# Kernel tuning notes

Hardware: AMD Instinct MI355X
Metric: run time of the kernel (lower is better)

Reference implementation:

```python
import jax, jax.numpy as jnp
import numpy as np

D_MODEL = 1024
N_SH = 16            # sub-heads per branch
N_BR = 4             # branches
H_TOT = N_BR * N_SH  # 64 total heads
DH = D_MODEL // N_SH # 64 head dim
BRANCH_CONFIGS = [(16, 0), (128, 16), (128, 0), (512, 144)]


def rms_norm(x):
    eps = jnp.finfo(x.dtype).eps
    return x * jax.lax.rsqrt(jnp.mean(x * x, axis=-1, keepdims=True) + eps)


def rope(x):
    # x: [B, H, T, Dh]; non-standard RoPE: even/odd split, halves concatenated
    T, Dh = x.shape[2], x.shape[3]
    inv_freq = 1.0 / (10000.0 ** (jnp.arange(0, Dh, 2, dtype=jnp.float32) / Dh))
    freqs = jnp.arange(T, dtype=jnp.float32)[:, None] * inv_freq[None, :]  # [T, Dh/2]
    cos = jnp.cos(freqs)[None, None]
    sin = jnp.sin(freqs)[None, None]
    x1 = x[..., 0::2]
    x2 = x[..., 1::2]
    return jnp.concatenate([-x2 * sin + x1 * cos, x1 * sin + x2 * cos], axis=-1)


def setup_inputs() -> dict:
    key = jax.random.key(0)
    ks = jax.random.split(key, 12)
    B, T, C = 2, 1024, D_MODEL
    s = 0.02
    return {
        "X": jax.random.normal(ks[0], (B, T, C), jnp.float32),
        "WQ": jax.random.normal(ks[1], (C, H_TOT * DH), jnp.float32) * s,
        "bQ": jax.random.normal(ks[2], (H_TOT * DH,), jnp.float32) * s,
        "WK": jax.random.normal(ks[3], (C, C), jnp.float32) * s,
        "bK": jax.random.normal(ks[4], (C,), jnp.float32) * s,
        "WV": jax.random.normal(ks[5], (C, H_TOT * DH), jnp.float32) * s,
        "bV": jax.random.normal(ks[6], (H_TOT * DH,), jnp.float32) * s,
        "WO": jax.random.normal(ks[7], (C, C), jnp.float32) * s,
        "bO": jax.random.normal(ks[8], (C,), jnp.float32) * s,
        "sink_scalars": jax.random.normal(ks[9], (H_TOT,), jnp.float32) * s,
        "v_nulls": jax.random.normal(ks[10], (H_TOT, DH), jnp.float32) * s,
    }


def reference(X, WQ, bQ, WK, bK, WV, bV, WO, bO, sink_scalars, v_nulls):
    B, T, C = X.shape
    # projections -> [B, H, T, Dh]
    q = (X @ WQ + bQ).reshape(B, T, H_TOT, DH).transpose(0, 2, 1, 3)
    q = rope(rms_norm(q))
    v = (X @ WV + bV).reshape(B, T, H_TOT, DH).transpose(0, 2, 1, 3)
    k = rope((X @ WK + bK).reshape(B, T, N_SH, DH).transpose(0, 2, 1, 3))
    k = jnp.tile(k, (1, N_BR, 1, 1))  # [B, H_TOT, T, Dh]

    # KMax scores with key self-norm denominator
    scores = jnp.einsum('bhqd,bhkd->bhqk', q, k)
    denom = jnp.sqrt(jnp.sum(k * k, axis=-1))[:, :, None, :]  # [B,H,1,T]
    w = scores / denom

    # banded masks per branch; note: off-band logits become 0 (NOT -inf) -> exp(0)=1 in softmax
    idx = jnp.arange(T)
    dist = idx[:, None] - idx[None, :]  # query - key
    bmasks = jnp.stack([((dist >= g) & (dist < h)).astype(w.dtype)
                        for (h, g) in BRANCH_CONFIGS], axis=0)  # [N_BR,T,T]
    full_mask = jnp.repeat(bmasks, N_SH, axis=0)[None]  # [1,H_TOT,T,T] (band subset of tril)
    w = w * full_mask

    # learnable tanh sink logit per head, concatenated as extra column
    sinks = jnp.broadcast_to(jnp.tanh(sink_scalars).reshape(1, H_TOT, 1, 1), (B, H_TOT, T, 1))
    probs = jax.nn.softmax(jnp.concatenate([w, sinks], axis=-1), axis=-1)

    out = jnp.einsum('bhqk,bhkd->bhqd', probs[..., :T], v)
    out = out + probs[..., T:] * v_nulls.reshape(1, H_TOT, 1, DH)

    # [B,H_TOT,T,Dh] -> [B,N_BR,T,C]
    ctx = out.reshape(B, N_BR, N_SH, T, DH).transpose(0, 1, 3, 2, 4).reshape(B, N_BR, T, C)
    y = ctx @ WO + bO
    return y.mean(axis=1)
```

## Files before the change

### kernel.cpp

```cpp
#include <hip/hip_runtime.h>
#include <hip/hip_bf16.h>
#include <math.h>

#define T_SEQ 1024
#define LOG2_10000 13.287712379549449f

typedef unsigned short u16;
typedef unsigned int u32;
typedef __attribute__((ext_vector_type(8))) short bf16x8;
typedef __attribute__((ext_vector_type(4))) float f32x4;

__device__ __forceinline__ void gload16(const u16* g, const u16* s) {
  __builtin_amdgcn_global_load_lds(
      (const __attribute__((address_space(1))) void*)g,
      (__attribute__((address_space(3))) void*)s, 16, 0, 0);
}

__device__ __forceinline__ u16 f2bf(float x) {
  __hip_bfloat16 h = __float2bfloat16(x);
  return *reinterpret_cast<u16*>(&h);
}
__device__ __forceinline__ float bf2f(u16 x) {
  __hip_bfloat16 h = *reinterpret_cast<__hip_bfloat16*>(&x);
  return __bfloat162float(h);
}

__device__ __forceinline__ void transpose_step(
    const float* __restrict__ W, u16* __restrict__ Wt, int N, int nbx,
    int local, int t, float (*tile)[33]) {
  int bx = local % nbx, by = local / nbx;
  int n0 = bx * 32, k0 = by * 32;
  int r = t >> 3, c4 = (t & 7) * 4;
  float4 v = *reinterpret_cast<const float4*>(&W[(size_t)(k0 + r) * N + n0 + c4]);
  tile[r][c4 + 0] = v.x;
  tile[r][c4 + 1] = v.y;
  tile[r][c4 + 2] = v.z;
  tile[r][c4 + 3] = v.w;
  __syncthreads();
  u16 o[4];
#pragma unroll
  for (int i = 0; i < 4; ++i) o[i] = f2bf(tile[c4 + i][r]);
  *reinterpret_cast<uint2*>(&Wt[(size_t)(n0 + r) * 1024 + k0 + c4]) =
      *reinterpret_cast<const uint2*>(o);
}

__global__ __launch_bounds__(256) void prep_kernel(
    const float* __restrict__ X, const float* __restrict__ WQ,
    const float* __restrict__ WK, const float* __restrict__ WV,
    const float* __restrict__ WO, const float* __restrict__ bQ,
    const float* __restrict__ bV, const float* __restrict__ bK,
    u16* __restrict__ Xb, u16* __restrict__ WQVKt, u16* __restrict__ WOt,
    float* __restrict__ bQVK, float* __restrict__ ctab, float* __restrict__ stab)
{
  __shared__ float tile[32][33];
  const int blk = blockIdx.x, t = threadIdx.x;
  if (blk < 128) {
    int id = blk * 256 + t;
    int tt = id >> 5, p = id & 31;
    float invf = exp2f(-LOG2_10000 * (float)(2 * p) * (1.0f / 64.0f));
    float ang = (float)tt * invf;
    float sn, cs;
    sincosf(ang, &sn, &cs);
    ctab[id] = cs;
    stab[id] = sn;
  } else if (blk < 1152) {
    int i = (blk - 128) * 256 + t;
    float4 a = reinterpret_cast<const float4*>(X)[2 * i];
    float4 b = reinterpret_cast<const float4*>(X)[2 * i + 1];
    u16 o[8] = {f2bf(a.x), f2bf(a.y), f2bf(a.z), f2bf(a.w),
                f2bf(b.x), f2bf(b.y), f2bf(b.z), f2bf(b.w)};
    reinterpret_cast<uint4*>(Xb)[i] = *reinterpret_cast<const uint4*>(o);
  } else if (blk < 5248) {
    transpose_step(WQ, WQVKt, 4096, 128, blk - 1152, t, tile);
  } else if (blk < 9344) {
    transpose_step(WV, WQVKt + (size_t)4096 * 1024, 4096, 128, blk - 5248, t, tile);
  } else if (blk < 10368) {
    transpose_step(WK, WQVKt + (size_t)8192 * 1024, 1024, 32, blk - 9344, t, tile);
  } else if (blk < 11392) {
    transpose_step(WO, WOt, 1024, 32, blk - 10368, t, tile);
  } else {
    int id = (blk - 11392) * 256 + t;
    if (id < 9216)
      bQVK[id] = (id < 4096) ? bQ[id] : (id < 8192) ? bV[id - 4096] : bK[id - 8192];
  }
}

__global__ __launch_bounds__(512, 4) void gemm_qv_kernel(
    const u16* __restrict__ Ab, const u16* __restrict__ Bt,
    const float* __restrict__ bias, u16* __restrict__ Cqv)
{
  __shared__ __align__(16) u16 sA[3][256 * 32];
  __shared__ __align__(16) u16 sB[3][128 * 32];

  const int tid = threadIdx.x;
  const int lane = tid & 63;
  const int w = tid >> 6;
  const int wm = w >> 2, wn = w & 3;
  const int l15 = lane & 15, l4 = lane >> 4;

  const int orig = blockIdx.x;
  const int xcd = orig & 7, j = orig >> 3;
  const int bx = xcd * 8 + (j & 7);
  const int by = j >> 3;
  const int m0 = by * 256, n0 = bx * 128;

  const int rA0 = tid >> 2, cA = tid & 3;
  const int scA = cA ^ ((rA0 >> 1) & 3);
  const int rB0 = tid >> 2;
  const int scB = cA ^ ((rB0 >> 1) & 3);
  const u16* aA0 = Ab + (size_t)(m0 + rA0) * 1024 + 8 * scA;
  const u16* aA1 = Ab + (size_t)(m0 + rA0 + 128) * 1024 + 8 * scA;
  const u16* aB0 = Bt + (size_t)(n0 + rB0) * 1024 + 8 * scB;

  const int cp = l4 ^ ((l15 >> 1) & 3);

  f32x4 acc[8][2];
#pragma unroll
  for (int i = 0; i < 8; ++i)
#pragma unroll
    for (int jn = 0; jn < 2; ++jn) acc[i][jn] = (f32x4){0.f, 0.f, 0.f, 0.f};

#define STAGE(t)                                                               \
  {                                                                            \
    const int sl = (t) % 3;                                                    \
    const int ko = (t) * 32;                                                   \
    gload16(aA0 + ko, &sA[sl][tid * 8]);                                       \
    gload16(aA1 + ko, &sA[sl][4096 + tid * 8]);                                \
    gload16(aB0 + ko, &sB[sl][tid * 8]);                                       \
  }

  STAGE(0);
#pragma unroll 1
  for (int t = 0; t < 32; ++t) {
    if (t + 1 < 32) {
      STAGE(t + 1);
      asm volatile("s_waitcnt vmcnt(3)" ::: "memory");
    } else {
      asm volatile("s_waitcnt vmcnt(0)" ::: "memory");
    }
    __builtin_amdgcn_sched_barrier(0);
    __builtin_amdgcn_s_barrier();
    __builtin_amdgcn_sched_barrier(0);

    const u16* tA = sA[t % 3];
    const u16* tB = sB[t % 3];

    bf16x8 bf[2];
#pragma unroll
    for (int n = 0; n < 2; ++n) {
      int row = wn * 32 + n * 16 + l15;
      bf[n] = *reinterpret_cast<const bf16x8*>(&tB[row * 32 + cp * 8]);
    }
    bf16x8 af[8];
#pragma unroll
    for (int m = 0; m < 8; ++m) {
      int row = wm * 128 + m * 16 + l15;
      af[m] = *reinterpret_cast<const bf16x8*>(&tA[row * 32 + cp * 8]);
    }
    __builtin_amdgcn_s_setprio(1);
#pragma unroll
    for (int m = 0; m < 8; ++m)
#pragma unroll
      for (int n = 0; n < 2; ++n)
        acc[m][n] = __builtin_amdgcn_mfma_f32_16x16x32_bf16(
            af[m], bf[n], acc[m][n], 0, 0, 0);
    __builtin_amdgcn_s_setprio(0);
  }
#undef STAGE

#pragma unroll
  for (int n = 0; n < 2; ++n) {
    int col = n0 + wn * 32 + n * 16 + l15;
    float bv = bias[col];
#pragma unroll
    for (int mf = 0; mf < 8; ++mf) {
#pragma unroll
      for (int r = 0; r < 4; ++r) {
        int row = m0 + wm * 128 + mf * 16 + l4 * 4 + r;
        Cqv[(size_t)row * 8192 + col] = f2bf(acc[mf][n][r] + bv);
      }
    }
  }
}

template <bool BF16OUT>
__global__ __launch_bounds__(256) void gemm64_kernel(
    const u16* __restrict__ Ab, const u16* __restrict__ Bt,
    const float* __restrict__ bias, void* __restrict__ Cv,
    int M, int N, int K)
{
  __shared__ __align__(16) u16 sA[2][64 * 64];
  __shared__ __align__(16) u16 sB[2][64 * 64];
  const int tid = threadIdx.x;
  const int lane = tid & 63;
  const int wv = tid >> 6;
  const int wm = wv >> 1, wn = wv & 1;
  const int l15 = lane & 15, l4 = lane >> 4;
  const int m0 = blockIdx.y * 64, n0 = blockIdx.x * 64;

  f32x4 acc[2][2];
#pragma unroll
  for (int i = 0; i < 2; ++i)
#pragma unroll
    for (int j = 0; j < 2; ++j) acc[i][j] = (f32x4){0.f, 0.f, 0.f, 0.f};

  const int r0s = tid >> 3,         c0s = tid & 7;
  const int r1s = (256 + tid) >> 3, c1s = (256 + tid) & 7;
  const int sc0 = c0s ^ (r0s & 7);
  const int sc1 = c1s ^ (r1s & 7);
  const u16* aA0 = Ab + (size_t)(m0 + r0s) * K + 8 * sc0;
  const u16* aA1 = Ab + (size_t)(m0 + r1s) * K + 8 * sc1;
  const u16* aB0 = Bt + (size_t)(n0 + r0s) * K + 8 * sc0;
  const u16* aB1 = Bt + (size_t)(n0 + r1s) * K + 8 * sc1;

  gload16(aA0, &sA[0][tid * 8]);
  gload16(aA1, &sA[0][2048 + tid * 8]);
  gload16(aB0, &sB[0][tid * 8]);
  gload16(aB1, &sB[0][2048 + tid * 8]);

  const int niter = K >> 6;
#pragma unroll 1
  for (int it = 0; it < niter; ++it) {
    const int buf = it & 1;
    __builtin_amdgcn_s_barrier();
    if (it + 1 < niter) {
      const int ko = (it + 1) * 64;
      gload16(aA0 + ko, &sA[buf ^ 1][tid * 8]);
      gload16(aA1 + ko, &sA[buf ^ 1][2048 + tid * 8]);
      gload16(aB0 + ko, &sB[buf ^ 1][tid * 8]);
      gload16(aB1 + ko, &sB[buf ^ 1][2048 + tid * 8]);
      asm volatile("s_waitcnt vmcnt(4)" ::: "memory");
    } else {
      asm volatile("s_waitcnt vmcnt(0)" ::: "memory");
    }
    __builtin_amdgcn_sched_barrier(0);
    bf16x8 af[2][2], bfv[2][2];
#pragma unroll
    for (int kk = 0; kk < 2; ++kk) {
#pragma unroll
      for (int mi = 0; mi < 2; ++mi) {
        int row = wm * 32 + mi * 16 + l15;
        int cs = (kk * 4 + l4) ^ (row & 7);
        af[mi][kk] = *reinterpret_cast<const bf16x8*>(&sA[buf][row * 64 + cs * 8]);
      }
#pragma unroll
      for (int ni = 0; ni < 2; ++ni) {
        int row = wn * 32 + ni * 16 + l15;
        int cs = (kk * 4 + l4) ^ (row & 7);
        bfv[ni][kk] = *reinterpret_cast<const bf16x8*>(&sB[buf][row * 64 + cs * 8]);
      }
    }
#pragma unroll
    for (int kk = 0; kk < 2; ++kk)
#pragma unroll
      for (int mi = 0; mi < 2; ++mi)
#pragma unroll
        for (int ni = 0; ni < 2; ++ni)
          acc[mi][ni] = __builtin_amdgcn_mfma_f32_16x16x32_bf16(
              af[mi][kk], bfv[ni][kk], acc[mi][ni], 0, 0, 0);
  }

#pragma unroll
  for (int mi = 0; mi < 2; ++mi)
#pragma unroll
    for (int ni = 0; ni < 2; ++ni) {
      int col = n0 + wn * 32 + ni * 16 + l15;
      float bv = bias[col];
#pragma unroll
      for (int r = 0; r < 4; ++r) {
        int row = m0 + wm * 32 + mi * 16 + l4 * 4 + r;
        float val = acc[mi][ni][r] + bv;
        size_t idx = (size_t)row * N + col;
        if (BF16OUT) ((u16*)Cv)[idx] = f2bf(val);
        else ((float*)Cv)[idx] = val;
      }
    }
}

__global__ __launch_bounds__(256) void qkvt_kernel(
    u16* __restrict__ QVbf, u16* __restrict__ Kbf,
    const float* __restrict__ ctab, const float* __restrict__ stab,
    float* __restrict__ part)
{
  const int blk = blockIdx.x;
  if (blk < 20480) {
    const int rid  = blk * 8 + (threadIdx.x >> 5);
    const int lane = threadIdx.x & 63;
    const int p    = lane & 31;
    const int gb   = lane & 32;

    u16* row;
    int t;
    const bool isQ = rid < 131072;
    if (isQ) {
      int h = rid & 63, bt = rid >> 6;
      t = bt & 1023;
      row = QVbf + (size_t)bt * 8192 + h * 64;
    } else {
      int r2 = rid - 131072;
      int hsL = r2 & 15, bt = r2 >> 4;
      t = bt & 1023;
      row = Kbf + (size_t)bt * 1024 + hsL * 64;
    }

    u32 v = reinterpret_cast<const u32*>(row)[p];
    float x1 = bf2f((u16)v), x2 = bf2f((u16)(v >> 16));
    float cs = ctab[t * 32 + p], sn = stab[t * 32 + p];

    float o_lo, o_hi;
    if (isQ) {
      float ss = x1 * x1 + x2 * x2;
      ss += __shfl_xor(ss, 1, 64);
      ss += __shfl_xor(ss, 2, 64);
      ss += __shfl_xor(ss, 4, 64);
      ss += __shfl_xor(ss, 8, 64);
      ss += __shfl_xor(ss, 16, 64);
      float rs = rsqrtf(ss * (1.0f / 64.0f) + 1.1920929e-7f);
      float xn1 = x1 * rs, xn2 = x2 * rs;
      o_lo = xn1 * cs - xn2 * sn;
      o_hi = xn1 * sn + xn2 * cs;
    } else {
      float xr1 = x1 * cs - x2 * sn;
      float xr2 = x1 * sn + x2 * cs;
      float ss = xr1 * xr1 + xr2 * xr2;
      ss += __shfl_xor(ss, 1, 64);
      ss += __shfl_xor(ss, 2, 64);
      ss += __shfl_xor(ss, 4, 64);
      ss += __shfl_xor(ss, 8, 64);
      ss += __shfl_xor(ss, 16, 64);
      float rs = rsqrtf(ss);
      o_lo = xr1 * rs;
      o_hi = xr2 * rs;
    }

    int m = (2 * p) & 31;
    float slo0 = __shfl(o_lo, gb + m, 64);
    float slo1 = __shfl(o_lo, gb + m + 1, 64);
    float shi0 = __shfl(o_hi, gb + m, 64);
    float shi1 = __shfl(o_hi, gb + m + 1, 64);
    float e0 = (p < 16) ? slo0 : shi0;
    float e1 = (p < 16) ? slo1 : shi1;
    reinterpret_cast<u32*>(row)[p] = (u32)f2bf(e0) | ((u32)f2bf(e1) << 16);
  } else {
    int vb = blk - 20480;
    int b = vb >> 6, ch = vb & 63;
    const u16* base = QVbf + (size_t)(b * 1024 + ch * 16) * 8192 + 4096;
#pragma unroll
    for (int g = 0; g < 2; ++g) {
      int c0 = (threadIdx.x + g * 256) * 8;
      float s[8] = {0.f, 0.f, 0.f, 0.f, 0.f, 0.f, 0.f, 0.f};
#pragma unroll 4
      for (int r = 0; r < 16; ++r) {
        bf16x8 v = *reinterpret_cast<const bf16x8*>(&base[(size_t)r * 8192 + c0]);
#pragma unroll
        for (int e = 0; e < 8; ++e) s[e] += bf2f((u16)v[e]);
      }
      float* dst = &part[(size_t)vb * 4096 + c0];
#pragma unroll
      for (int e = 0; e < 8; ++e) dst[e] = s[e];
    }
  }
}

__global__ __launch_bounds__(256) void vsum_reduce_kernel(
    const float* __restrict__ part, float* __restrict__ Vsum) {
  int id = blockIdx.x * 256 + threadIdx.x;
  int b = id >> 12, n = id & 4095;
  float s = 0.f;
#pragma unroll 8
  for (int ch = 0; ch < 64; ++ch) s += part[(size_t)(b * 64 + ch) * 4096 + n];
  Vsum[id] = s;
}

__global__ __launch_bounds__(256) void attn_mfma_kernel(
    const u16* __restrict__ Qv, const u16* __restrict__ Kb,
    const float* __restrict__ Vsum, const float* __restrict__ sink,
    const float* __restrict__ vnull, u16* __restrict__ mctxb)
{
  __shared__ __align__(16) u16 sQ[64 * 64];
  __shared__ __align__(16) u16 sK[2][64 * 64];
  __shared__ __align__(16) u16 sVt[2][64 * 64];
  __shared__ __align__(16) u16 sP[64 * 64];

  int blk = blockIdx.x;
  blk = (blk & 7) * 64 + (blk >> 3);
  const int qt  = blk & 15;
  const int hs  = (blk >> 4) & 15;
  const int b   = blk >> 8;
  const int qt0 = qt * 64;

  const int tid  = threadIdx.x;
  const int lane = tid & 63;
  const int wv   = tid >> 6;
  const int l15  = lane & 15;
  const int l4   = lane >> 4;
  const int qr0  = tid >> 3, qi0 = tid & 7;
  const int qr1  = qr0 + 32;
  const int vjp  = tid & 31, vdg = tid >> 5;
  const int qrow = wv * 16 + l15;

  constexpr int HCFG[4] = {16, 128, 128, 512};
  constexpr int GCFG[4] = {0, 16, 0, 144};

  f32x4 macc[4];
#pragma unroll
  for (int i = 0; i < 4; ++i) macc[i] = (f32x4){0.f, 0.f, 0.f, 0.f};

#pragma unroll 1
  for (int br = 0; br < 4; ++br) {
    const int h = br * 16 + hs;
    const int hmax = HCFG[br], g = GCFG[br];
    int klo = qt0 - (hmax - 1); if (klo < 0) klo = 0;
    int khi = qt0 + 63 - g;     if (khi > 1023) khi = 1023;
    const int nc = (khi >= klo) ? ((khi - klo) / 64 + 1) : 0;

    gload16(Qv + (size_t)(b * 1024 + qt0 + qr0) * 8192 + h * 64 + 8 * (qi0 ^ (qr0 & 7)),
            sQ + (size_t)wv * 512);
    gload16(Qv + (size_t)(b * 1024 + qt0 + qr1) * 8192 + h * 64 + 8 * (qi0 ^ (qr1 & 7)),
            sQ + 2048 + (size_t)wv * 512);
    bf16x8 va, vb;
    if (nc > 0) {
      int ja0 = klo + qr0; if (ja0 > 1023) ja0 = 1023;
      int ja1 = klo + qr1; if (ja1 > 1023) ja1 = 1023;
      gload16(Kb + (size_t)(b * 1024 + ja0) * 1024 + hs * 64 + 8 * (qi0 ^ (qr0 & 7)),
              sK[0] + (size_t)wv * 512);
      gload16(Kb + (size_t)(b * 1024 + ja1) * 1024 + hs * 64 + 8 * (qi0 ^ (qr1 & 7)),
              sK[0] + 2048 + (size_t)wv * 512);
      int jva = klo + 2 * vjp, jvb = jva + 1;
      if (jva > 1023) jva = 1023;
      if (jvb > 1023) jvb = 1023;
      va = *reinterpret_cast<const bf16x8*>(
          &Qv[(size_t)(b * 1024 + jva) * 8192 + 4096 + h * 64 + vdg * 8]);
      vb = *reinterpret_cast<const bf16x8*>(
          &Qv[(size_t)(b * 1024 + jvb) * 8192 + 4096 + h * 64 + vdg * 8]);
    }
    asm volatile("s_waitcnt vmcnt(0)" ::: "memory");
    __builtin_amdgcn_sched_barrier(0);
    if (nc > 0) {
#pragma unroll
      for (int e = 0; e < 8; ++e) {
        int d = vdg * 8 + e;
        u32 pack = (u32)(u16)va[e] | ((u32)(u16)vb[e] << 16);
        *reinterpret_cast<u32*>(
            (char*)sVt[0] + d * 128 + ((4 * vjp) ^ ((d & 7) << 4))) = pack;
      }
    }
    asm volatile("s_waitcnt lgkmcnt(0)" ::: "memory");
    __builtin_amdgcn_sched_barrier(0);
    __builtin_amdgcn_s_barrier();

    bf16x8 afQ[2];
#pragma unroll
    for (int kh = 0; kh < 2; ++kh) {
      int cs = (4 * kh + l4) ^ (l15 & 7);
      afQ[kh] = *reinterpret_cast<const bf16x8*>(&sQ[qrow * 64 + cs * 8]);
    }

    f32x4 outv[4];
#pragma unroll
    for (int i = 0; i < 4; ++i) outv[i] = (f32x4){0.f, 0.f, 0.f, 0.f};
    float zacc[4] = {0.f, 0.f, 0.f, 0.f};

    int buf = 0;
#pragma unroll 1
    for (int c = 0; c < nc; ++c) {
      const int j0 = klo + c * 64;
      const bool nxt = (c + 1 < nc);
      if (nxt) {
        int j0n = j0 + 64;
        int ja0 = j0n + qr0; if (ja0 > 1023) ja0 = 1023;
        int ja1 = j0n + qr1; if (ja1 > 1023) ja1 = 1023;
        gload16(Kb + (size_t)(b * 1024 + ja0) * 1024 + hs * 64 + 8 * (qi0 ^ (qr0 & 7)),
                sK[buf ^ 1] + (size_t)wv * 512);
        gload16(Kb + (size_t)(b * 1024 + ja1) * 1024 + hs * 64 + 8 * (qi0 ^ (qr1 & 7)),
                sK[buf ^ 1] + 2048 + (size_t)wv * 512);
        int jva = j0n + 2 * vjp, jvb = jva + 1;
        if (jva > 1023) jva = 1023;
        if (jvb > 1023) jvb = 1023;
        va = *reinterpret_cast<const bf16x8*>(
            &Qv[(size_t)(b * 1024 + jva) * 8192 + 4096 + h * 64 + vdg * 8]);
        vb = *reinterpret_cast<const bf16x8*>(
            &Qv[(size_t)(b * 1024 + jvb) * 8192 + 4096 + h * 64 + vdg * 8]);
      }
      f32x4 sfr[4];
      __builtin_amdgcn_s_setprio(1);
#pragma unroll
      for (int jt = 0; jt < 4; ++jt) {
        int krow = jt * 16 + l15;
        f32x4 acc = (f32x4){0.f, 0.f, 0.f, 0.f};
#pragma unroll
        for (int kh = 0; kh < 2; ++kh) {
          int cs = (4 * kh + l4) ^ (l15 & 7);
          bf16x8 bk = *reinterpret_cast<const bf16x8*>(&sK[buf][krow * 64 + cs * 8]);
          acc = __builtin_amdgcn_mfma_f32_16x16x32_bf16(afQ[kh], bk, acc, 0, 0, 0);
        }
        sfr[jt] = acc;
      }
      __builtin_amdgcn_s_setprio(0);
#pragma unroll
      for (int jt = 0; jt < 4; ++jt) {
        int jloc = jt * 16 + l15;
        int jabs = j0 + jloc;
#pragma unroll
        for (int r = 0; r < 4; ++r) {
          int q_r = wv * 16 + l4 * 4 + r;
          int dist = (qt0 + q_r) - jabs;
          bool inband = (dist >= g) & (dist < hmax) & (jabs < 1024);
          float pv = inband ? (__expf(sfr[jt][r]) - 1.0f) : 0.0f;
          zacc[r] += pv;
          *reinterpret_cast<u16*>(
              (char*)sP + q_r * 128 + ((2 * jloc) ^ ((q_r & 7) << 4))) = f2bf(pv);
        }
      }
      asm volatile("s_waitcnt lgkmcnt(0)" ::: "memory");
      __builtin_amdgcn_sched_barrier(0);
      bf16x8 afP[2];
#pragma unroll
      for (int kh = 0; kh < 2; ++kh) {
        int cs = (4 * kh + l4) ^ (l15 & 7);
        afP[kh] = *reinterpret_cast<const bf16x8*>(&sP[qrow * 64 + cs * 8]);
      }
      __builtin_amdgcn_s_setprio(1);
#pragma unroll
      for (int dt = 0; dt < 4; ++dt) {
        int drow = dt * 16 + l15;
#pragma unroll
        for (int kh = 0; kh < 2; ++kh) {
          int cs = (4 * kh + l4) ^ (l15 & 7);
          bf16x8 bv = *reinterpret_cast<const bf16x8*>(&sVt[buf][drow * 64 + cs * 8]);
          outv[dt] = __builtin_amdgcn_mfma_f32_16x16x32_bf16(afP[kh], bv, outv[dt], 0, 0, 0);
        }
      }
      __builtin_amdgcn_s_setprio(0);
      if (nxt) {
#pragma unroll
        for (int e = 0; e < 8; ++e) {
          int d = vdg * 8 + e;
          u32 pack = (u32)(u16)va[e] | ((u32)(u16)vb[e] << 16);
          *reinterpret_cast<u32*>(
              (char*)sVt[buf ^ 1] + d * 128 + ((4 * vjp) ^ ((d & 7) << 4))) = pack;
        }
      }
      asm volatile("s_waitcnt vmcnt(0) lgkmcnt(0)" ::: "memory");
      __builtin_amdgcn_sched_barrier(0);
      __builtin_amdgcn_s_barrier();
      buf ^= 1;
    }

#pragma unroll
    for (int r = 0; r < 4; ++r) {
      zacc[r] += __shfl_xor(zacc[r], 1, 64);
      zacc[r] += __shfl_xor(zacc[r], 2, 64);
      zacc[r] += __shfl_xor(zacc[r], 4, 64);
      zacc[r] += __shfl_xor(zacc[r], 8, 64);
    }
    float es = __expf(tanhf(sink[h]));
#pragma unroll
    for (int dt = 0; dt < 4; ++dt) {
      int d = dt * 16 + l15;
      float vs = Vsum[(size_t)b * 4096 + h * 64 + d];
      float vn = vnull[h * 64 + d];
#pragma unroll
      for (int r = 0; r < 4; ++r) {
        float invZ = 1.0f / (1024.0f + zacc[r] + es);
        macc[dt][r] += (outv[dt][r] + vs + es * vn) * invZ;
      }
    }
  }

#pragma unroll
  for (int dt = 0; dt < 4; ++dt) {
#pragma unroll
    for (int r = 0; r < 4; ++r) {
      int q_r = wv * 16 + l4 * 4 + r;
      mctxb[(size_t)(b * 1024 + qt0 + q_r) * 1024 + hs * 64 + dt * 16 + l15] =
          f2bf(0.25f * macc[dt][r]);
    }
  }
}

extern "C" void kernel_launch(void* const* d_in, const int* in_sizes, int n_in,
                              void* d_out, int out_size, void* d_ws, size_t ws_size,
                              hipStream_t stream) {
  (void)in_sizes; (void)n_in; (void)out_size; (void)ws_size;
  const float* X    = (const float*)d_in[0];
  const float* WQ   = (const float*)d_in[1];
  const float* bQ   = (const float*)d_in[2];
  const float* WK   = (const float*)d_in[3];
  const float* bK   = (const float*)d_in[4];
  const float* WV   = (const float*)d_in[5];
  const float* bV   = (const float*)d_in[6];
  const float* WO   = (const float*)d_in[7];
  const float* bO   = (const float*)d_in[8];
  const float* sink = (const float*)d_in[9];
  const float* vnul = (const float*)d_in[10];
  float* Y = (float*)d_out;

  char* p = (char*)d_ws;
  u16*   Xb    = (u16*)p;   p += (size_t)2048 * 1024 * 2;
  u16*   WQVKt = (u16*)p;   p += (size_t)9216 * 1024 * 2;
  u16*   WOt   = (u16*)p;   p += (size_t)1024 * 1024 * 2;
  u16*   QVbf  = (u16*)p;   p += (size_t)2048 * 8192 * 2;
  u16*   Kbf   = (u16*)p;   p += (size_t)2048 * 1024 * 2;
  u16*   mctxb = (u16*)p;   p += (size_t)2048 * 1024 * 2;
  float* Vsum  = (float*)p; p += (size_t)2 * 4096 * 4;
  float* vpart = (float*)p; p += (size_t)128 * 4096 * 4;
  float* bQVK  = (float*)p; p += (size_t)9216 * 4;
  float* ctab  = (float*)p; p += (size_t)32768 * 4;
  float* stab  = (float*)p; p += (size_t)32768 * 4;

  dim3 blk(256);
  prep_kernel<<<11428, blk, 0, stream>>>(X, WQ, WK, WV, WO, bQ, bV, bK,
                                         Xb, WQVKt, WOt, bQVK, ctab, stab);

  gemm_qv_kernel<<<512, dim3(512), 0, stream>>>(Xb, WQVKt, bQVK, QVbf);
  gemm64_kernel<true><<<dim3(16, 32), blk, 0, stream>>>(
      Xb, WQVKt + (size_t)8192 * 1024, bQVK + 8192, Kbf, 2048, 1024, 1024);

  qkvt_kernel<<<20608, blk, 0, stream>>>(QVbf, Kbf, ctab, stab, vpart);
  vsum_reduce_kernel<<<32, blk, 0, stream>>>(vpart, Vsum);

  attn_mfma_kernel<<<512, blk, 0, stream>>>(QVbf, Kbf, Vsum, sink, vnul, mctxb);

  gemm64_kernel<false><<<dim3(16, 32), blk, 0, stream>>>(mctxb, WOt, bO, Y, 2048, 1024, 1024);
}
```

Measured before the change: 132.2 us.

## Split attention across branches into separate blocks with a merge kernel

The attention kernel now launches one block per (batch, head-slot, query tile, branch) instead of looping over all four branches inside a block. That gives four times as many blocks and better load balance across CUs, since branch 3 has far more key chunks than the others. Each block writes its per-branch bf16 partial to a new workspace buffer, and a separate merge kernel sums the four partials into the context. The cost is an extra launch, extra global memory traffic, and one more bf16 rounding step before the sum.

```diff
diff --git a/kernel.cpp b/kernel.cpp
--- a/kernel.cpp
+++ b/kernel.cpp
@@ -375,7 +375,7 @@
 __global__ __launch_bounds__(256) void attn_mfma_kernel(
     const u16* __restrict__ Qv, const u16* __restrict__ Kb,
     const float* __restrict__ Vsum, const float* __restrict__ sink,
-    const float* __restrict__ vnull, u16* __restrict__ mctxb)
+    const float* __restrict__ vnull, u16* __restrict__ mpart)
 {
   __shared__ __align__(16) u16 sQ[64 * 64];
   __shared__ __align__(16) u16 sK[2][64 * 64];
@@ -383,10 +383,11 @@
   __shared__ __align__(16) u16 sP[64 * 64];
 
   int blk = blockIdx.x;
-  blk = (blk & 7) * 64 + (blk >> 3);
-  const int qt  = blk & 15;
-  const int hs  = (blk >> 4) & 15;
-  const int b   = blk >> 8;
+  blk = (blk & 7) * 256 + (blk >> 3);
+  const int br  = blk & 3;
+  const int qt  = (blk >> 2) & 15;
+  const int hs  = (blk >> 6) & 15;
+  const int b   = blk >> 10;
   const int qt0 = qt * 64;
 
   const int tid  = threadIdx.x;
@@ -402,31 +403,73 @@
   constexpr int HCFG[4] = {16, 128, 128, 512};
   constexpr int GCFG[4] = {0, 16, 0, 144};
 
-  f32x4 macc[4];
-#pragma unroll
-  for (int i = 0; i < 4; ++i) macc[i] = (f32x4){0.f, 0.f, 0.f, 0.f};
-
+  const int h = br * 16 + hs;
+  const int hmax = HCFG[br], g = GCFG[br];
+  int klo = qt0 - (hmax - 1); if (klo < 0) klo = 0;
+  int khi = qt0 + 63 - g;     if (khi > 1023) khi = 1023;
+  const int nc = (khi >= klo) ? ((khi - klo) / 64 + 1) : 0;
+
+  gload16(Qv + (size_t)(b * 1024 + qt0 + qr0) * 8192 + h * 64 + 8 * (qi0 ^ (qr0 & 7)),
+          sQ + (size_t)wv * 512);
+  gload16(Qv + (size_t)(b * 1024 + qt0 + qr1) * 8192 + h * 64 + 8 * (qi0 ^ (qr1 & 7)),
+          sQ + 2048 + (size_t)wv * 512);
+  bf16x8 va, vb;
+  if (nc > 0) {
+    int ja0 = klo + qr0; if (ja0 > 1023) ja0 = 1023;
+    int ja1 = klo + qr1; if (ja1 > 1023) ja1 = 1023;
+    gload16(Kb + (size_t)(b * 1024 + ja0) * 1024 + hs * 64 + 8 * (qi0 ^ (qr0 & 7)),
+            sK[0] + (size_t)wv * 512);
+    gload16(Kb + (size_t)(b * 1024 + ja1) * 1024 + hs * 64 + 8 * (qi0 ^ (qr1 & 7)),
+            sK[0] + 2048 + (size_t)wv * 512);
+    int jva = klo + 2 * vjp, jvb = jva + 1;
+    if (jva > 1023) jva = 1023;
+    if (jvb > 1023) jvb = 1023;
+    va = *reinterpret_cast<const bf16x8*>(
+        &Qv[(size_t)(b * 1024 + jva) * 8192 + 4096 + h * 64 + vdg * 8]);
+    vb = *reinterpret_cast<const bf16x8*>(
+        &Qv[(size_t)(b * 1024 + jvb) * 8192 + 4096 + h * 64 + vdg * 8]);
+  }
+  asm volatile("s_waitcnt vmcnt(0)" ::: "memory");
+  __builtin_amdgcn_sched_barrier(0);
+  if (nc > 0) {
+#pragma unroll
+    for (int e = 0; e < 8; ++e) {
+      int d = vdg * 8 + e;
+      u32 pack = (u32)(u16)va[e] | ((u32)(u16)vb[e] << 16);
+      *reinterpret_cast<u32*>(
+          (char*)sVt[0] + d * 128 + ((4 * vjp) ^ ((d & 7) << 4))) = pack;
+    }
+  }
+  asm volatile("s_waitcnt lgkmcnt(0)" ::: "memory");
+  __builtin_amdgcn_sched_barrier(0);
+  __builtin_amdgcn_s_barrier();
+
+  bf16x8 afQ[2];
+#pragma unroll
+  for (int kh = 0; kh < 2; ++kh) {
+    int cs = (4 * kh + l4) ^ (l15 & 7);
+    afQ[kh] = *reinterpret_cast<const bf16x8*>(&sQ[qrow * 64 + cs * 8]);
+  }
+
+  f32x4 outv[4];
+#pragma unroll
+  for (int i = 0; i < 4; ++i) outv[i] = (f32x4){0.f, 0.f, 0.f, 0.f};
+  float zacc[4] = {0.f, 0.f, 0.f, 0.f};
+
+  int buf = 0;
 #pragma unroll 1
-  for (int br = 0; br < 4; ++br) {
-    const int h = br * 16 + hs;
-    const int hmax = HCFG[br], g = GCFG[br];
-    int klo = qt0 - (hmax - 1); if (klo < 0) klo = 0;
-    int khi = qt0 + 63 - g;     if (khi > 1023) khi = 1023;
-    const int nc = (khi >= klo) ? ((khi - klo) / 64 + 1) : 0;
-
-    gload16(Qv + (size_t)(b * 1024 + qt0 + qr0) * 8192 + h * 64 + 8 * (qi0 ^ (qr0 & 7)),
-            sQ + (size_t)wv * 512);
-    gload16(Qv + (size_t)(b * 1024 + qt0 + qr1) * 8192 + h * 64 + 8 * (qi0 ^ (qr1 & 7)),
-            sQ + 2048 + (size_t)wv * 512);
-    bf16x8 va, vb;
-    if (nc > 0) {
-      int ja0 = klo + qr0; if (ja0 > 1023) ja0 = 1023;
-      int ja1 = klo + qr1; if (ja1 > 1023) ja1 = 1023;
+  for (int c = 0; c < nc; ++c) {
+    const int j0 = klo + c * 64;
+    const bool nxt = (c + 1 < nc);
+    if (nxt) {
+      int j0n = j0 + 64;
+      int ja0 = j0n + qr0; if (ja0 > 1023) ja0 = 1023;
+      int ja1 = j0n + qr1; if (ja1 > 1023) ja1 = 1023;
       gload16(Kb + (size_t)(b * 1024 + ja0) * 1024 + hs * 64 + 8 * (qi0 ^ (qr0 & 7)),
-              sK[0] + (size_t)wv * 512);
+              sK[buf ^ 1] + (size_t)wv * 512);
       gload16(Kb + (size_t)(b * 1024 + ja1) * 1024 + hs * 64 + 8 * (qi0 ^ (qr1 & 7)),
-              sK[0] + 2048 + (size_t)wv * 512);
-      int jva = klo + 2 * vjp, jvb = jva + 1;
+              sK[buf ^ 1] + 2048 + (size_t)wv * 512);
+      int jva = j0n + 2 * vjp, jvb = jva + 1;
       if (jva > 1023) jva = 1023;
       if (jvb > 1023) jvb = 1023;
       va = *reinterpret_cast<const bf16x8*>(
@@ -434,149 +477,112 @@
       vb = *reinterpret_cast<const bf16x8*>(
           &Qv[(size_t)(b * 1024 + jvb) * 8192 + 4096 + h * 64 + vdg * 8]);
     }
-    asm volatile("s_waitcnt vmcnt(0)" ::: "memory");
+    f32x4 sfr[4];
+    __builtin_amdgcn_s_setprio(1);
+#pragma unroll
+    for (int jt = 0; jt < 4; ++jt) {
+      int krow = jt * 16 + l15;
+      f32x4 acc = (f32x4){0.f, 0.f, 0.f, 0.f};
+#pragma unroll
+      for (int kh = 0; kh < 2; ++kh) {
+        int cs = (4 * kh + l4) ^ (l15 & 7);
+        bf16x8 bk = *reinterpret_cast<const bf16x8*>(&sK[buf][krow * 64 + cs * 8]);
+        acc = __builtin_amdgcn_mfma_f32_16x16x32_bf16(afQ[kh], bk, acc, 0, 0, 0);
+      }
+      sfr[jt] = acc;
+    }
+    __builtin_amdgcn_s_setprio(0);
+#pragma unroll
+    for (int jt = 0; jt < 4; ++jt) {
+      int jloc = jt * 16 + l15;
+      int jabs = j0 + jloc;
+#pragma unroll
+      for (int r = 0; r < 4; ++r) {
+        int q_r = wv * 16 + l4 * 4 + r;
+        int dist = (qt0 + q_r) - jabs;
+        bool inband = (dist >= g) & (dist < hmax) & (jabs < 1024);
+        float pv = inband ? (__expf(sfr[jt][r]) - 1.0f) : 0.0f;
+        zacc[r] += pv;
+        *reinterpret_cast<u16*>(
+            (char*)sP + q_r * 128 + ((2 * jloc) ^ ((q_r & 7) << 4))) = f2bf(pv);
+      }
+    }
+    asm volatile("s_waitcnt lgkmcnt(0)" ::: "memory");
     __builtin_amdgcn_sched_barrier(0);
-    if (nc > 0) {
+    bf16x8 afP[2];
+#pragma unroll
+    for (int kh = 0; kh < 2; ++kh) {
+      int cs = (4 * kh + l4) ^ (l15 & 7);
+      afP[kh] = *reinterpret_cast<const bf16x8*>(&sP[qrow * 64 + cs * 8]);
+    }
+    __builtin_amdgcn_s_setprio(1);
+#pragma unroll
+    for (int dt = 0; dt < 4; ++dt) {
+      int drow = dt * 16 + l15;
+#pragma unroll
+      for (int kh = 0; kh < 2; ++kh) {
+        int cs = (4 * kh + l4) ^ (l15 & 7);
+        bf16x8 bv = *reinterpret_cast<const bf16x8*>(&sVt[buf][drow * 64 + cs * 8]);
+        outv[dt] = __builtin_amdgcn_mfma_f32_16x16x32_bf16(afP[kh], bv, outv[dt], 0, 0, 0);
+      }
+    }
+    __builtin_amdgcn_s_setprio(0);
+    if (nxt) {
 #pragma unroll
       for (int e = 0; e < 8; ++e) {
         int d = vdg * 8 + e;
         u32 pack = (u32)(u16)va[e] | ((u32)(u16)vb[e] << 16);
         *reinterpret_cast<u32*>(
-            (char*)sVt[0] + d * 128 + ((4 * vjp) ^ ((d & 7) << 4))) = pack;
-      }
-    }
-    asm volatile("s_waitcnt lgkmcnt(0)" ::: "memory");
+            (char*)sVt[buf ^ 1] + d * 128 + ((4 * vjp) ^ ((d & 7) << 4))) = pack;
+      }
+    }
+    asm volatile("s_waitcnt vmcnt(0) lgkmcnt(0)" ::: "memory");
     __builtin_amdgcn_sched_barrier(0);
     __builtin_amdgcn_s_barrier();
-
-    bf16x8 afQ[2];
-#pragma unroll
-    for (int kh = 0; kh < 2; ++kh) {
-      int cs = (4 * kh + l4) ^ (l15 & 7);
-      afQ[kh] = *reinterpret_cast<const bf16x8*>(&sQ[qrow * 64 + cs * 8]);
-    }
-
-    f32x4 outv[4];
-#pragma unroll
-    for (int i = 0; i < 4; ++i) outv[i] = (f32x4){0.f, 0.f, 0.f, 0.f};
-    float zacc[4] = {0.f, 0.f, 0.f, 0.f};
-
-    int buf = 0;
-#pragma unroll 1
-    for (int c = 0; c < nc; ++c) {
-      const int j0 = klo + c * 64;
-      const bool nxt = (c + 1 < nc);
-      if (nxt) {
-        int j0n = j0 + 64;
-        int ja0 = j0n + qr0; if (ja0 > 1023) ja0 = 1023;
-        int ja1 = j0n + qr1; if (ja1 > 1023) ja1 = 1023;
-        gload16(Kb + (size_t)(b * 1024 + ja0) * 1024 + hs * 64 + 8 * (qi0 ^ (qr0 & 7)),
-                sK[buf ^ 1] + (size_t)wv * 512);
-        gload16(Kb + (size_t)(b * 1024 + ja1) * 1024 + hs * 64 + 8 * (qi0 ^ (qr1 & 7)),
-                sK[buf ^ 1] + 2048 + (size_t)wv * 512);
-        int jva = j0n + 2 * vjp, jvb = jva + 1;
-        if (jva > 1023) jva = 1023;
-        if (jvb > 1023) jvb = 1023;
-        va = *reinterpret_cast<const bf16x8*>(
-            &Qv[(size_t)(b * 1024 + jva) * 8192 + 4096 + h * 64 + vdg * 8]);
-        vb = *reinterpret_cast<const bf16x8*>(
-            &Qv[(size_t)(b * 1024 + jvb) * 8192 + 4096 + h * 64 + vdg * 8]);
-      }
-      f32x4 sfr[4];
-      __builtin_amdgcn_s_setprio(1);
-#pragma unroll
-      for (int jt = 0; jt < 4; ++jt) {
-        int krow = jt * 16 + l15;
-        f32x4 acc = (f32x4){0.f, 0.f, 0.f, 0.f};
-#pragma unroll
-        for (int kh = 0; kh < 2; ++kh) {
-          int cs = (4 * kh + l4) ^ (l15 & 7);
-          bf16x8 bk = *reinterpret_cast<const bf16x8*>(&sK[buf][krow * 64 + cs * 8]);
-          acc = __builtin_amdgcn_mfma_f32_16x16x32_bf16(afQ[kh], bk, acc, 0, 0, 0);
-        }
-        sfr[jt] = acc;
-      }
-      __builtin_amdgcn_s_setprio(0);
-#pragma unroll
-      for (int jt = 0; jt < 4; ++jt) {
-        int jloc = jt * 16 + l15;
-        int jabs = j0 + jloc;
-#pragma unroll
-        for (int r = 0; r < 4; ++r) {
-          int q_r = wv * 16 + l4 * 4 + r;
-          int dist = (qt0 + q_r) - jabs;
-          bool inband = (dist >= g) & (dist < hmax) & (jabs < 1024);
-          float pv = inband ? (__expf(sfr[jt][r]) - 1.0f) : 0.0f;
-          zacc[r] += pv;
-          *reinterpret_cast<u16*>(
-              (char*)sP + q_r * 128 + ((2 * jloc) ^ ((q_r & 7) << 4))) = f2bf(pv);
-        }
-      }
-      asm volatile("s_waitcnt lgkmcnt(0)" ::: "memory");
-      __builtin_amdgcn_sched_barrier(0);
-      bf16x8 afP[2];
-#pragma unroll
-      for (int kh = 0; kh < 2; ++kh) {
-        int cs = (4 * kh + l4) ^ (l15 & 7);
-        afP[kh] = *reinterpret_cast<const bf16x8*>(&sP[qrow * 64 + cs * 8]);
-      }
-      __builtin_amdgcn_s_setprio(1);
-#pragma unroll
-      for (int dt = 0; dt < 4; ++dt) {
-        int drow = dt * 16 + l15;
-#pragma unroll
-        for (int kh = 0; kh < 2; ++kh) {
-          int cs = (4 * kh + l4) ^ (l15 & 7);
-          bf16x8 bv = *reinterpret_cast<const bf16x8*>(&sVt[buf][drow * 64 + cs * 8]);
-          outv[dt] = __builtin_amdgcn_mfma_f32_16x16x32_bf16(afP[kh], bv, outv[dt], 0, 0, 0);
-        }
-      }
-      __builtin_amdgcn_s_setprio(0);
-      if (nxt) {
-#pragma unroll
-        for (int e = 0; e < 8; ++e) {
-          int d = vdg * 8 + e;
-          u32 pack = (u32)(u16)va[e] | ((u32)(u16)vb[e] << 16);
-          *reinterpret_cast<u32*>(
-              (char*)sVt[buf ^ 1] + d * 128 + ((4 * vjp) ^ ((d & 7) << 4))) = pack;
-        }
-      }
-      asm volatile("s_waitcnt vmcnt(0) lgkmcnt(0)" ::: "memory");
-      __builtin_amdgcn_sched_barrier(0);
-      __builtin_amdgcn_s_barrier();
-      buf ^= 1;
-    }
-
-#pragma unroll
-    for (int r = 0; r < 4; ++r) {
-      zacc[r] += __shfl_xor(zacc[r], 1, 64);
-      zacc[r] += __shfl_xor(zacc[r], 2, 64);
-      zacc[r] += __shfl_xor(zacc[r], 4, 64);
-      zacc[r] += __shfl_xor(zacc[r], 8, 64);
-    }
-    float es = __expf(tanhf(sink[h]));
-#pragma unroll
-    for (int dt = 0; dt < 4; ++dt) {
-      int d = dt * 16 + l15;
-      float vs = Vsum[(size_t)b * 4096 + h * 64 + d];
-      float vn = vnull[h * 64 + d];
-#pragma unroll
-      for (int r = 0; r < 4; ++r) {
-        float invZ = 1.0f / (1024.0f + zacc[r] + es);
-        macc[dt][r] += (outv[dt][r] + vs + es * vn) * invZ;
-      }
-    }
-  }
-
+    buf ^= 1;
+  }
+
+#pragma unroll
+  for (int r = 0; r < 4; ++r) {
+    zacc[r] += __shfl_xor(zacc[r], 1, 64);
+    zacc[r] += __shfl_xor(zacc[r], 2, 64);
+    zacc[r] += __shfl_xor(zacc[r], 4, 64);
+    zacc[r] += __shfl_xor(zacc[r], 8, 64);
+  }
+  float es = __expf(tanhf(sink[h]));
+  u16* mp = mpart + (size_t)br * 2048 * 1024;
 #pragma unroll
   for (int dt = 0; dt < 4; ++dt) {
+    int d = dt * 16 + l15;
+    float vs = Vsum[(size_t)b * 4096 + h * 64 + d];
+    float vn = vnull[h * 64 + d];
 #pragma unroll
     for (int r = 0; r < 4; ++r) {
       int q_r = wv * 16 + l4 * 4 + r;
-      mctxb[(size_t)(b * 1024 + qt0 + q_r) * 1024 + hs * 64 + dt * 16 + l15] =
-          f2bf(0.25f * macc[dt][r]);
-    }
-  }
+      float invZ = 1.0f / (1024.0f + zacc[r] + es);
+      mp[(size_t)(b * 1024 + qt0 + q_r) * 1024 + hs * 64 + d] =
+          f2bf(0.25f * (outv[dt][r] + vs + es * vn) * invZ);
+    }
+  }
+}
+
+__global__ __launch_bounds__(256) void merge_kernel(
+    const u16* __restrict__ mpart, u16* __restrict__ mctxb) {
+  const size_t id = (size_t)blockIdx.x * 256 + threadIdx.x;
+  const size_t off = id * 8;
+  const size_t stride = (size_t)2048 * 1024;
+  bf16x8 p0 = *reinterpret_cast<const bf16x8*>(&mpart[off]);
+  bf16x8 p1 = *reinterpret_cast<const bf16x8*>(&mpart[stride + off]);
+  bf16x8 p2 = *reinterpret_cast<const bf16x8*>(&mpart[2 * stride + off]);
+  bf16x8 p3 = *reinterpret_cast<const bf16x8*>(&mpart[3 * stride + off]);
+  u16 o[8];
+#pragma unroll
+  for (int e = 0; e < 8; ++e) {
+    float s = (bf2f((u16)p0[e]) + bf2f((u16)p1[e])) +
+              (bf2f((u16)p2[e]) + bf2f((u16)p3[e]));
+    o[e] = f2bf(s);
+  }
+  *reinterpret_cast<uint4*>(&mctxb[off]) = *reinterpret_cast<const uint4*>(o);
 }
 
 extern "C" void kernel_launch(void* const* d_in, const int* in_sizes, int n_in,
@@ -603,6 +609,7 @@
   u16*   QVbf  = (u16*)p;   p += (size_t)2048 * 8192 * 2;
   u16*   Kbf   = (u16*)p;   p += (size_t)2048 * 1024 * 2;
   u16*   mctxb = (u16*)p;   p += (size_t)2048 * 1024 * 2;
+  u16*   mpart = (u16*)p;   p += (size_t)4 * 2048 * 1024 * 2;
   float* Vsum  = (float*)p; p += (size_t)2 * 4096 * 4;
   float* vpart = (float*)p; p += (size_t)128 * 4096 * 4;
   float* bQVK  = (float*)p; p += (size_t)9216 * 4;
@@ -620,7 +627,8 @@
   qkvt_kernel<<<20608, blk, 0, stream>>>(QVbf, Kbf, ctab, stab, vpart);
   vsum_reduce_kernel<<<32, blk, 0, stream>>>(vpart, Vsum);
 
-  attn_mfma_kernel<<<512, blk, 0, stream>>>(QVbf, Kbf, Vsum, sink, vnul, mctxb);
+  attn_mfma_kernel<<<2048, blk, 0, stream>>>(QVbf, Kbf, Vsum, sink, vnul, mpart);
+  merge_kernel<<<1024, blk, 0, stream>>>(mpart, mctxb);
 
   gemm64_kernel<false><<<dim3(16, 32), blk, 0, stream>>>(mctxb, WOt, bO, Y, 2048, 1024, 1024);
 }
```

Result: slower. 140.2 us (+6.0%).
